# Kernel tuning notes

Hardware: AMD Instinct MI355X
Metric: run time of the kernel (lower is better)

The kernel has to match this reference:

```python
import jax, jax.numpy as jnp
import numpy as np

DEPTH = 4
EPS = 1e-5


def _bn(x, g, b):
    # training-mode BatchNorm over (B,H,W) per channel
    m = x.mean(axis=(0, 2, 3), keepdims=True)
    v = x.var(axis=(0, 2, 3), keepdims=True)
    return (x - m) * jax.lax.rsqrt(v + EPS) * g[None, :, None, None] + b[None, :, None, None]


def _conv_bn(x, w, g, b):
    # 1x1 conv (no bias) + BatchNorm
    y = jnp.einsum('bchw,oc->bohw', x, w)
    return _bn(y, g, b)


def _block_max_broadcast(x, gsz):
    # max over each (H/gsz, W/gsz) block of a gsz x gsz grid, broadcast back
    B, C, H, W = x.shape
    xr = x.reshape(B, C, gsz, H // gsz, gsz, W // gsz)
    m = xr.max(axis=(3, 5), keepdims=True)
    return jnp.broadcast_to(m, xr.shape).reshape(B, C, H, W)


def setup_inputs() -> dict:
    key = jax.random.key(0)
    ks = jax.random.split(key, 3)
    B, C, H, W = 4, 128, 256, 256
    x = jax.random.normal(ks[0], (B, C, H, W), dtype=jnp.float32)
    conv_w = jax.random.normal(ks[1], (DEPTH, C, C), dtype=jnp.float32) * 0.05
    conv_g = jnp.ones((DEPTH, C), dtype=jnp.float32)
    conv_b = jnp.zeros((DEPTH, C), dtype=jnp.float32)
    final_w = jax.random.normal(ks[2], (C, (DEPTH + 1) * C), dtype=jnp.float32) * 0.05
    final_g = jnp.ones((C,), dtype=jnp.float32)
    final_b = jnp.zeros((C,), dtype=jnp.float32)
    return {"x": x, "conv_w": conv_w, "conv_g": conv_g, "conv_b": conv_b,
            "final_w": final_w, "final_g": final_g, "final_b": final_b}


def reference(x, conv_w, conv_g, conv_b, final_w, final_g, final_b):
    # p[0]: identity; p[1+d]: block-max over 2^d x 2^d grid broadcast back, then 1x1 conv+BN
    p = [x]
    for d in range(DEPTH):
        pooled = _block_max_broadcast(x, 2 ** d)  # d=0 -> global max broadcast
        p.append(_conv_bn(pooled, conv_w[d], conv_g[d], conv_b[d]))
    out = jnp.concatenate(p, axis=1)  # [B, 5C, H, W]
    return _conv_bn(out, final_w, final_g, final_b)
```

## Files before the change

kernel.cpp:

```cpp
#include <hip/hip_runtime.h>
#include <hip/hip_bf16.h>
#include <math.h>
#include <float.h>

#define B_ 4
#define C_ 128
#define P_ 65536

#define M3_OFF      0
#define M2_OFF      32768
#define M1_OFF      40960
#define M0_OFF      43008
#define YBASE_      43520
#define SCALED_OFF  87040
#define SHIFTD_OFF  87552
#define CONTRIB_OFF 88064
#define S3_OFF      120832
#define SX_OFF      153600
#define G_OFF       154112
#define SCALEF_OFF  219648
#define SHIFTF_OFF  219776
#define MAXP_OFF    219904
#define SUMP_OFF    744192

using short8 = __attribute__((ext_vector_type(8))) short;
using f32x4 = __attribute__((ext_vector_type(4))) float;
using f32x16 = __attribute__((ext_vector_type(16))) float;

__device__ __forceinline__ int level_rel(int d) {
    return YBASE_ - 512 * (((1 << (2 * (d + 1))) - 1) / 3);
}

__device__ __forceinline__ unsigned int bfpair(float a, float b) {
    union { __hip_bfloat162 h2; unsigned int u; } cv;
    cv.h2 = __float22bfloat162_rn(make_float2(a, b));
    return cv.u;
}

#define GLDS16(src, dst)                                                    \
    __builtin_amdgcn_global_load_lds(                                       \
        (const __attribute__((address_space(1))) unsigned int*)(src),       \
        (__attribute__((address_space(3))) unsigned int*)(dst), 16, 0, 0)

__global__ __launch_bounds__(512, 4) void k_gram_pool(const float* __restrict__ x,
                                                      float* __restrict__ ws,
                                                      float* __restrict__ gpart) {
    __shared__ float buf[4][4096];
    int wg = blockIdx.x;
    int b = wg >> 7, rc = wg & 127;
    const float* xb = x + (size_t)b * C_ * P_ + (size_t)rc * 512;
    int t_ = threadIdx.x, l = t_ & 63, wv = t_ >> 6;
    int qi = wv & 3;
    int qjb = (wv >> 2) * 2;
    bool doacc = (wv < 4);
    int lrow = l >> 3, lch = l & 7;

    f32x16 acc[2];
#pragma unroll
    for (int j = 0; j < 2; ++j)
#pragma unroll
        for (int r = 0; r < 16; ++r) acc[j][r] = 0.f;
    float mxA[8], smA[8];
#pragma unroll
    for (int j = 0; j < 8; ++j) { mxA[j] = -FLT_MAX; smA[j] = 0.f; }

#define ISSUE(tt)                                                            \
    do {                                                                     \
        _Pragma("unroll") for (int i_ = 0; i_ < 2; ++i_) {                   \
            int row_ = wv * 16 + i_ * 8 + lrow;                              \
            int ch_ = lch ^ (row_ & 7);                                      \
            GLDS16(xb + (size_t)row_ * P_ + (tt) * 32 + ch_ * 4,             \
                   &buf[(tt) & 3][(wv * 16 + i_ * 8) * 32]);                 \
        }                                                                    \
    } while (0)

    ISSUE(0);
    ISSUE(1);
    ISSUE(2);

#pragma unroll
    for (int t = 0; t < 16; ++t) {
        if (t <= 13)
            asm volatile("s_waitcnt vmcnt(4)" ::: "memory");
        else if (t == 14)
            asm volatile("s_waitcnt vmcnt(2)" ::: "memory");
        else
            asm volatile("s_waitcnt vmcnt(0)" ::: "memory");
        __builtin_amdgcn_sched_barrier(0);
        __builtin_amdgcn_s_barrier();
        asm volatile("" ::: "memory");
        __builtin_amdgcn_sched_barrier(0);
        if (t + 3 < 16) ISSUE(t + 3);

        const float* tl = &buf[t & 3][0];
        int jc = t & 7;
#pragma unroll
        for (int ks = 0; ks < 2; ++ks) {
            int ch = ks * 4 + ((l >> 5) << 1);
            short8 fa;
            {
                int row = qi * 32 + (l & 31);
                int sw = row & 7;
                float4 v0 = *(const float4*)(tl + row * 32 + ((ch ^ sw) << 2));
                float4 v1 = *(const float4*)(tl + row * 32 + (((ch + 1) ^ sw) << 2));
                if (doacc) {
                    mxA[jc] = fmaxf(mxA[jc],
                        fmaxf(fmaxf(fmaxf(v0.x, v0.y), fmaxf(v0.z, v0.w)),
                              fmaxf(fmaxf(v1.x, v1.y), fmaxf(v1.z, v1.w))));
                    smA[jc] += ((v0.x + v0.y) + (v0.z + v0.w)) +
                               ((v1.x + v1.y) + (v1.z + v1.w));
                }
                union { uint4 u; short8 s8; } cu;
                cu.u = make_uint4(bfpair(v0.x, v0.y), bfpair(v0.z, v0.w),
                                  bfpair(v1.x, v1.y), bfpair(v1.z, v1.w));
                fa = cu.s8;
            }
#pragma unroll
            for (int j = 0; j < 2; ++j) {
                int row = (qjb + j) * 32 + (l & 31);
                int sw = row & 7;
                float4 v0 = *(const float4*)(tl + row * 32 + ((ch ^ sw) << 2));
                float4 v1 = *(const float4*)(tl + row * 32 + (((ch + 1) ^ sw) << 2));
                union { uint4 u; short8 s8; } cu;
                cu.u = make_uint4(bfpair(v0.x, v0.y), bfpair(v0.z, v0.w),
                                  bfpair(v1.x, v1.y), bfpair(v1.z, v1.w));
                acc[j] = __builtin_amdgcn_mfma_f32_32x32x16_bf16(fa, cu.s8, acc[j], 0, 0, 0);
            }
        }
    }
#undef ISSUE

    size_t gb = (size_t)wg * 16384;
#pragma unroll
    for (int j = 0; j < 2; ++j)
#pragma unroll
        for (int r = 0; r < 16; ++r) {
            int row = qi * 32 + (r & 3) + 8 * (r >> 2) + 4 * (l >> 5);
            int col = (qjb + j) * 32 + (l & 31);
            gpart[gb + (size_t)row * 128 + col] = acc[j][r];
        }
    if (doacc) {
        int i3 = rc >> 4, rr = rc & 15;
#pragma unroll
        for (int jc = 0; jc < 8; ++jc) {
            float m = mxA[jc], sv = smA[jc];
            m = fmaxf(m, __shfl_xor(m, 32));
            sv += __shfl_xor(sv, 32);
            if (l < 32) {
                int c = qi * 32 + l;
                size_t idx = ((size_t)(b * 128 + c) * 64 + i3 * 8 + jc) * 16 + rr;
                ws[MAXP_OFF + idx] = m;
                ws[SUMP_OFF + idx] = sv;
            }
        }
    }
}

__global__ __launch_bounds__(256) void k_reduceG(const float* __restrict__ gpart,
                                                 float* __restrict__ ws) {
    int tid = blockIdx.x * 256 + threadIdx.x;
    int b = tid >> 14, inner = tid & 16383;
    const float* p = gpart + (size_t)b * 128 * 16384 + inner;
    float s = 0.f;
    for (int r = 0; r < 128; ++r) s += p[(size_t)r * 16384];
    ws[G_OFF + tid] = s;
}

__global__ __launch_bounds__(256) void k_reduceMS(float* __restrict__ ws) {
    int bc = blockIdx.x;
    int t = threadIdx.x;
    int blk = t >> 2, q = t & 3;
    __shared__ float bm[64], bs[64];
    __shared__ float lv[24];
    __shared__ float sxr[8];
    {
        size_t base = (size_t)bc * 1024 + blk * 16 + q * 4;
        float4 mv = *(const float4*)(ws + MAXP_OFF + base);
        float4 sv = *(const float4*)(ws + SUMP_OFF + base);
        float m = fmaxf(fmaxf(mv.x, mv.y), fmaxf(mv.z, mv.w));
        float s = (sv.x + sv.y) + (sv.z + sv.w);
        m = fmaxf(m, __shfl_xor(m, 1)); s += __shfl_xor(s, 1);
        m = fmaxf(m, __shfl_xor(m, 2)); s += __shfl_xor(s, 2);
        if (q == 0) {
            bm[blk] = m;
            bs[blk] = s;
            ws[M3_OFF + (size_t)bc * 64 + blk] = m;
            ws[S3_OFF + (size_t)bc * 64 + blk] = s;
        }
    }
    __syncthreads();
    if (t < 8) {
        float sx = 0.f;
        for (int r = 0; r < 8; ++r) sx += bs[t * 8 + r];
        sxr[t] = sx;
    }
    if (t < 16) {
        int i2 = t >> 2, j2 = t & 3;
        float m = -FLT_MAX;
        for (int a = 0; a < 2; ++a)
            for (int b2 = 0; b2 < 2; ++b2)
                m = fmaxf(m, bm[(2 * i2 + a) * 8 + 2 * j2 + b2]);
        lv[t] = m;
        ws[M2_OFF + (size_t)bc * 16 + t] = m;
    }
    __syncthreads();
    if (t == 0) {
        float sx = 0.f;
        for (int r = 0; r < 8; ++r) sx += sxr[r];
        ws[SX_OFF + bc] = sx;
    }
    if (t < 4) {
        int i1 = t >> 1, j1 = t & 1;
        float m = -FLT_MAX;
        for (int a = 0; a < 2; ++a)
            for (int b2 = 0; b2 < 2; ++b2)
                m = fmaxf(m, lv[(2 * i1 + a) * 4 + 2 * j1 + b2]);
        lv[16 + t] = m;
        ws[M1_OFF + (size_t)bc * 4 + t] = m;
    }
    __syncthreads();
    if (t == 0)
        ws[M0_OFF + bc] = fmaxf(fmaxf(lv[16], lv[17]), fmaxf(lv[18], lv[19]));
}

__global__ __launch_bounds__(256) void k_conv_pool(const float* __restrict__ conv_w,
                                                   float* __restrict__ ws) {
    int bid = blockIdx.x;
    int d = bid >> 4, b = (bid >> 2) & 3, cchunk = bid & 3;
    int NB = 1 << (2 * d);
    int rel = level_rel(d);
    const float* Mb = ws + rel + (size_t)b * 128 * NB;
    float* Yb = ws + YBASE_ + rel + (size_t)b * 128 * NB;
    __shared__ float mlds[8192];
    int t = threadIdx.x;
    int tot = 128 * NB;
    for (int i = t; i < tot; i += 256) mlds[i] = Mb[i];
    __syncthreads();
    if (NB >= 4) {
        int nbq = NB >> 2;
        int nq = 32 * nbq;
        for (int qi = t; qi < nq; qi += 256) {
            int co = cchunk * 32 + (qi >> (2 * d - 2));
            int bq = qi & (nbq - 1);
            const float* wrow = conv_w + ((size_t)d * 128 + co) * 128;
            float a0 = 0.f, a1 = 0.f, a2 = 0.f, a3 = 0.f;
            for (int ci = 0; ci < 128; ++ci) {
                float4 mv = *(const float4*)(&mlds[ci * NB + bq * 4]);
                float wvv = wrow[ci];
                a0 = fmaf(wvv, mv.x, a0);
                a1 = fmaf(wvv, mv.y, a1);
                a2 = fmaf(wvv, mv.z, a2);
                a3 = fmaf(wvv, mv.w, a3);
            }
            float4 r;
            r.x = a0; r.y = a1; r.z = a2; r.w = a3;
            *(float4*)(&Yb[co * NB + bq * 4]) = r;
        }
    } else {
        for (int oi = t; oi < 32; oi += 256) {
            int co = cchunk * 32 + oi;
            const float* wrow = conv_w + (size_t)co * 128;
            float acc = 0.f;
            for (int ci = 0; ci < 128; ++ci) acc = fmaf(mlds[ci], wrow[ci], acc);
            Yb[co] = acc;
        }
    }
}

__global__ __launch_bounds__(256) void k_bnstats_d(const float* __restrict__ conv_g,
                                                   const float* __restrict__ conv_b,
                                                   float* __restrict__ ws) {
    int tid = blockIdx.x * 256 + threadIdx.x;
    if (tid >= 512) return;
    int d = tid >> 7, c = tid & 127;
    int NB = 1 << (2 * d);
    const float* Y = ws + YBASE_ + level_rel(d);
    int n = 4 * NB;
    float s = 0.f;
    for (int b = 0; b < 4; ++b)
        for (int k = 0; k < NB; ++k) s += Y[((size_t)b * 128 + c) * NB + k];
    float mean = s / (float)n;
    float v = 0.f;
    for (int b = 0; b < 4; ++b)
        for (int k = 0; k < NB; ++k) {
            float dd = Y[((size_t)b * 128 + c) * NB + k] - mean;
            v = fmaf(dd, dd, v);
        }
    float var = v / (float)n;
    float sc = conv_g[d * 128 + c] * rsqrtf(var + 1e-5f);
    ws[SCALED_OFF + tid] = sc;
    ws[SHIFTD_OFF + tid] = conv_b[d * 128 + c] - mean * sc;
}

__global__ __launch_bounds__(128) void k_contrib(const float* __restrict__ final_w,
                                                 float* __restrict__ ws) {
    int b = blockIdx.x >> 6, blk3 = blockIdx.x & 63;
    int i3 = blk3 >> 3, j3 = blk3 & 7;
    __shared__ float pn[512];
    int t = threadIdx.x;
    for (int k = t; k < 512; k += 128) {
        int d = k >> 7, c = k & 127;
        int sh = 3 - d;
        int blkd = (i3 >> sh) * (1 << d) + (j3 >> sh);
        int NB = 1 << (2 * d);
        float yv = ws[YBASE_ + level_rel(d) + ((size_t)b * 128 + c) * NB + blkd];
        pn[k] = yv * ws[SCALED_OFF + k] + ws[SHIFTD_OFF + k];
    }
    __syncthreads();
    const float* fw = final_w + (size_t)t * 640 + 128;
    float acc = 0.f;
#pragma unroll 8
    for (int k = 0; k < 512; k += 4) {
        float4 f = *(const float4*)(fw + k);
        acc = fmaf(pn[k], f.x, acc);
        acc = fmaf(pn[k + 1], f.y, acc);
        acc = fmaf(pn[k + 2], f.z, acc);
        acc = fmaf(pn[k + 3], f.w, acc);
    }
    ws[CONTRIB_OFF + ((size_t)b * 128 + t) * 64 + blk3] = acc;
}

__global__ __launch_bounds__(128) void k_stats(const float* __restrict__ final_w,
                                               const float* __restrict__ final_g,
                                               const float* __restrict__ final_b,
                                               float* __restrict__ ws) {
    int o = blockIdx.x, t = threadIdx.x;
    __shared__ __align__(16) float wlds[128];
    __shared__ __align__(16) float cvl[64];
    __shared__ float rbuf[4];
    wlds[t] = final_w[(size_t)o * 640 + t];
    __syncthreads();
    float SSQ = 0.f, SUM = 0.f;
    for (int b = 0; b < 4; ++b) {
        if (t < 64) cvl[t] = ws[CONTRIB_OFF + (size_t)(b * 128 + o) * 64 + t];
        __syncthreads();
        const float* Gb = ws + G_OFF + (size_t)b * 16384 + (size_t)t * 128;
        float a1 = 0.f;
#pragma unroll 8
        for (int k = 0; k < 128; k += 4) {
            float4 g = *(const float4*)(Gb + k);
            float4 w = *(const float4*)(&wlds[k]);
            a1 = fmaf(g.x, w.x, fmaf(g.y, w.y, fmaf(g.z, w.z, fmaf(g.w, w.w, a1))));
        }
        const float* S3p = ws + S3_OFF + (size_t)(b * 128 + t) * 64;
        float a2 = 0.f;
#pragma unroll 8
        for (int k = 0; k < 64; k += 4) {
            float4 sv = *(const float4*)(S3p + k);
            float4 cv = *(const float4*)(&cvl[k]);
            a2 = fmaf(sv.x, cv.x, fmaf(sv.y, cv.y, fmaf(sv.z, cv.z, fmaf(sv.w, cv.w, a2))));
        }
        float r1 = (a1 + 2.f * a2) * wlds[t];
        float r2 = wlds[t] * ws[SX_OFF + b * 128 + t];
        if (t < 64) {
            r1 += 1024.f * cvl[t] * cvl[t];
            r2 += 1024.f * cvl[t];
        }
#pragma unroll
        for (int k = 1; k < 64; k <<= 1) {
            r1 += __shfl_xor(r1, k);
            r2 += __shfl_xor(r2, k);
        }
        if ((t & 63) == 0) {
            rbuf[(t >> 6) * 2] = r1;
            rbuf[(t >> 6) * 2 + 1] = r2;
        }
        __syncthreads();
        SSQ += rbuf[0] + rbuf[2];
        SUM += rbuf[1] + rbuf[3];
        __syncthreads();
    }
    if (t == 0) {
        float mean = SUM / 262144.f;
        float var = SSQ / 262144.f - mean * mean;
        float sc = final_g[o] * rsqrtf(var + 1e-5f);
        ws[SCALEF_OFF + o] = sc;
        ws[SHIFTF_OFF + o] = final_b[o] - mean * sc;
    }
}

__global__ __launch_bounds__(256) void k_out(const float* __restrict__ x,
                                             const float* __restrict__ final_w,
                                             const float* __restrict__ ws,
                                             float* __restrict__ out) {
    __shared__ uint4 wtileq[2048];
    __shared__ float scl[128], shf[128], cvs[512];
    unsigned char* wtile = (unsigned char*)wtileq;
    int wgid = blockIdx.x;
    int b = wgid >> 9, pt = wgid & 511;
    int p0 = pt * 128;
    int t = threadIdx.x, l = t & 63, wv = t >> 6;
#pragma unroll
    for (int it = 0; it < 32; ++it) {
        int pid = it * 256 + t;
        int o = pid >> 6, cp = (pid & 63) * 2;
        float2 f = *(const float2*)(final_w + (size_t)o * 640 + cp);
        unsigned int u = bfpair(f.x, f.y);
        int wa = (o * 256 + cp * 2) ^ ((o & 7) << 4);
        *(unsigned int*)(wtile + wa) = u;
    }
    if (t < 128) {
        scl[t] = ws[SCALEF_OFF + t];
        shf[t] = ws[SHIFTF_OFF + t];
    }
    int i3 = pt >> 6, jb = (pt & 1) * 4;
    for (int q = t; q < 512; q += 256) {
        int o = q >> 2, jj = q & 3;
        cvs[q] = ws[CONTRIB_OFF + (size_t)(b * 128 + o) * 64 + i3 * 8 + jb + jj];
    }
    __syncthreads();

    const float* xb = x + (size_t)b * C_ * P_;
    int pw = p0 + wv * 32;
    f32x4 acc[8][2];
#pragma unroll
    for (int i = 0; i < 8; ++i) {
        acc[i][0] = (f32x4){0.f, 0.f, 0.f, 0.f};
        acc[i][1] = (f32x4){0.f, 0.f, 0.f, 0.f};
    }
#pragma unroll
    for (int ks = 0; ks < 4; ++ks) {
        short8 bf[2];
#pragma unroll
        for (int nt = 0; nt < 2; ++nt) {
            const float* xp = xb + (size_t)(ks * 32 + (l >> 4) * 8) * P_ + (pw + nt * 16 + (l & 15));
            float f0 = xp[0 * P_], f1 = xp[1 * P_], f2 = xp[2 * P_], f3 = xp[3 * P_];
            float f4 = xp[4 * P_], f5 = xp[5 * P_], f6 = xp[6 * P_], f7 = xp[7 * P_];
            union { uint4 u; short8 s; } cvtu;
            cvtu.u = make_uint4(bfpair(f0, f1), bfpair(f2, f3), bfpair(f4, f5), bfpair(f6, f7));
            bf[nt] = cvtu.s;
        }
#pragma unroll
        for (int mt = 0; mt < 8; ++mt) {
            int ra = ((mt * 16 + (l & 15)) * 256 + ks * 64 + (l >> 4) * 16) ^ ((l & 7) << 4);
            short8 af = *(const short8*)(wtile + ra);
            acc[mt][0] = __builtin_amdgcn_mfma_f32_16x16x32_bf16(af, bf[0], acc[mt][0], 0, 0, 0);
            acc[mt][1] = __builtin_amdgcn_mfma_f32_16x16x32_bf16(af, bf[1], acc[mt][1], 0, 0, 0);
        }
    }
#pragma unroll
    for (int mt = 0; mt < 8; ++mt)
#pragma unroll
        for (int nt = 0; nt < 2; ++nt) {
            int p = pw + nt * 16 + (l & 15);
            int jj = ((p & 255) >> 5) & 3;
#pragma unroll
            for (int r = 0; r < 4; ++r) {
                int o = mt * 16 + (l >> 4) * 4 + r;
                float z = acc[mt][nt][r] + cvs[o * 4 + jj];
                out[(size_t)(b * 128 + o) * P_ + p] = fmaf(z, scl[o], shf[o]);
            }
        }
}

extern "C" void kernel_launch(void* const* d_in, const int* in_sizes, int n_in,
                              void* d_out, int out_size, void* d_ws, size_t ws_size,
                              hipStream_t stream) {
    const float* x = (const float*)d_in[0];
    const float* conv_w = (const float*)d_in[1];
    const float* conv_g = (const float*)d_in[2];
    const float* conv_b = (const float*)d_in[3];
    const float* final_w = (const float*)d_in[4];
    const float* final_g = (const float*)d_in[5];
    const float* final_b = (const float*)d_in[6];
    float* out = (float*)d_out;
    float* ws = (float*)d_ws;

    k_gram_pool<<<512, 512, 0, stream>>>(x, ws, out);
    k_reduceG<<<256, 256, 0, stream>>>(out, ws);
    k_reduceMS<<<512, 256, 0, stream>>>(ws);
    k_conv_pool<<<64, 256, 0, stream>>>(conv_w, ws);
    k_bnstats_d<<<2, 256, 0, stream>>>(conv_g, conv_b, ws);
    k_contrib<<<B_ * 64, 128, 0, stream>>>(final_w, ws);
    k_stats<<<128, 128, 0, stream>>>(final_w, final_g, final_b, ws);
    k_out<<<2048, 256, 0, stream>>>(x, final_w, ws, out);
}
```

Baseline: 194.0 us.

## Convert tiles to bf16 once in registers before LDS staging in gram kernel

Replaces the async global-to-LDS fp32 pipeline with register loads that compute max/sum and convert to bf16 once, then store swizzled bf16 tiles into a double-buffered LDS. MFMA operands are read straight from LDS as short8, removing the repeated fp32 reads and bf16 conversions that every wave performed for its A and B fragments. The tile per phase grows to 128 columns (4 phases instead of 16), using register prefetch for overlap, which raises register pressure and drops the deeper async prefetch.

```diff
diff --git a/kernel.cpp b/kernel.cpp
--- a/kernel.cpp
+++ b/kernel.cpp
@@ -37,98 +37,78 @@
     return cv.u;
 }
 
-#define GLDS16(src, dst)                                                    \
-    __builtin_amdgcn_global_load_lds(                                       \
-        (const __attribute__((address_space(1))) unsigned int*)(src),       \
-        (__attribute__((address_space(3))) unsigned int*)(dst), 16, 0, 0)
-
 __global__ __launch_bounds__(512, 4) void k_gram_pool(const float* __restrict__ x,
                                                       float* __restrict__ ws,
                                                       float* __restrict__ gpart) {
-    __shared__ float buf[4][4096];
+    __shared__ __align__(16) unsigned short buf[2][16384];
     int wg = blockIdx.x;
     int b = wg >> 7, rc = wg & 127;
     const float* xb = x + (size_t)b * C_ * P_ + (size_t)rc * 512;
     int t_ = threadIdx.x, l = t_ & 63, wv = t_ >> 6;
     int qi = wv & 3;
     int qjb = (wv >> 2) * 2;
-    bool doacc = (wv < 4);
-    int lrow = l >> 3, lch = l & 7;
+    int srow = wv * 16 + (l >> 2);
+    int sq = l & 3;
+    const float* sp = xb + (size_t)srow * P_ + sq * 32;
 
     f32x16 acc[2];
 #pragma unroll
     for (int j = 0; j < 2; ++j)
 #pragma unroll
         for (int r = 0; r < 16; ++r) acc[j][r] = 0.f;
-    float mxA[8], smA[8];
-#pragma unroll
-    for (int j = 0; j < 8; ++j) { mxA[j] = -FLT_MAX; smA[j] = 0.f; }
-
-#define ISSUE(tt)                                                            \
+    float mxcb[2] = {-FLT_MAX, -FLT_MAX};
+    float smcb[2] = {0.f, 0.f};
+    float4 ld[8];
+
+#define SLOAD(ph)                                                            \
     do {                                                                     \
-        _Pragma("unroll") for (int i_ = 0; i_ < 2; ++i_) {                   \
-            int row_ = wv * 16 + i_ * 8 + lrow;                              \
-            int ch_ = lch ^ (row_ & 7);                                      \
-            GLDS16(xb + (size_t)row_ * P_ + (tt) * 32 + ch_ * 4,             \
-                   &buf[(tt) & 3][(wv * 16 + i_ * 8) * 32]);                 \
+        _Pragma("unroll") for (int k_ = 0; k_ < 8; ++k_)                     \
+            ld[k_] = *(const float4*)(sp + (ph) * 128 + k_ * 4);             \
+    } while (0)
+#define SSTORE(ph)                                                           \
+    do {                                                                     \
+        _Pragma("unroll") for (int k_ = 0; k_ < 8; ++k_) {                   \
+            float4 v_ = ld[k_];                                              \
+            mxcb[(ph) & 1] = fmaxf(mxcb[(ph) & 1],                           \
+                fmaxf(fmaxf(v_.x, v_.y), fmaxf(v_.z, v_.w)));                \
+            smcb[(ph) & 1] += (v_.x + v_.y) + (v_.z + v_.w);                 \
+        }                                                                    \
+        _Pragma("unroll") for (int k_ = 0; k_ < 4; ++k_) {                   \
+            uint4 u_ = make_uint4(                                           \
+                bfpair(ld[2 * k_].x, ld[2 * k_].y),                          \
+                bfpair(ld[2 * k_].z, ld[2 * k_].w),                          \
+                bfpair(ld[2 * k_ + 1].x, ld[2 * k_ + 1].y),                  \
+                bfpair(ld[2 * k_ + 1].z, ld[2 * k_ + 1].w));                 \
+            int ch_ = (sq * 4 + k_) ^ (srow & 7);                            \
+            *(uint4*)(&buf[(ph) & 1][srow * 128 + ch_ * 8]) = u_;            \
         }                                                                    \
     } while (0)
 
-    ISSUE(0);
-    ISSUE(1);
-    ISSUE(2);
-
-#pragma unroll
-    for (int t = 0; t < 16; ++t) {
-        if (t <= 13)
-            asm volatile("s_waitcnt vmcnt(4)" ::: "memory");
-        else if (t == 14)
-            asm volatile("s_waitcnt vmcnt(2)" ::: "memory");
-        else
-            asm volatile("s_waitcnt vmcnt(0)" ::: "memory");
-        __builtin_amdgcn_sched_barrier(0);
-        __builtin_amdgcn_s_barrier();
-        asm volatile("" ::: "memory");
-        __builtin_amdgcn_sched_barrier(0);
-        if (t + 3 < 16) ISSUE(t + 3);
-
-        const float* tl = &buf[t & 3][0];
-        int jc = t & 7;
-#pragma unroll
-        for (int ks = 0; ks < 2; ++ks) {
-            int ch = ks * 4 + ((l >> 5) << 1);
-            short8 fa;
-            {
-                int row = qi * 32 + (l & 31);
-                int sw = row & 7;
-                float4 v0 = *(const float4*)(tl + row * 32 + ((ch ^ sw) << 2));
-                float4 v1 = *(const float4*)(tl + row * 32 + (((ch + 1) ^ sw) << 2));
-                if (doacc) {
-                    mxA[jc] = fmaxf(mxA[jc],
-                        fmaxf(fmaxf(fmaxf(v0.x, v0.y), fmaxf(v0.z, v0.w)),
-                              fmaxf(fmaxf(v1.x, v1.y), fmaxf(v1.z, v1.w))));
-                    smA[jc] += ((v0.x + v0.y) + (v0.z + v0.w)) +
-                               ((v1.x + v1.y) + (v1.z + v1.w));
-                }
-                union { uint4 u; short8 s8; } cu;
-                cu.u = make_uint4(bfpair(v0.x, v0.y), bfpair(v0.z, v0.w),
-                                  bfpair(v1.x, v1.y), bfpair(v1.z, v1.w));
-                fa = cu.s8;
+    SLOAD(0);
+    SSTORE(0);
+    __syncthreads();
+
+#pragma unroll
+    for (int ph = 0; ph < 4; ++ph) {
+        if (ph < 3) SLOAD(ph + 1);
+        const unsigned short* tl = buf[ph & 1];
+#pragma unroll
+        for (int ks = 0; ks < 8; ++ks) {
+            int ch = ks * 2 + (l >> 5);
+            int rowa = qi * 32 + (l & 31);
+            short8 fa = *(const short8*)(tl + rowa * 128 + ((ch ^ (rowa & 7)) * 8));
+#pragma unroll
+            for (int j = 0; j < 2; ++j) {
+                int rowb = (qjb + j) * 32 + (l & 31);
+                short8 fb = *(const short8*)(tl + rowb * 128 + ((ch ^ (rowb & 7)) * 8));
+                acc[j] = __builtin_amdgcn_mfma_f32_32x32x16_bf16(fa, fb, acc[j], 0, 0, 0);
             }
-#pragma unroll
-            for (int j = 0; j < 2; ++j) {
-                int row = (qjb + j) * 32 + (l & 31);
-                int sw = row & 7;
-                float4 v0 = *(const float4*)(tl + row * 32 + ((ch ^ sw) << 2));
-                float4 v1 = *(const float4*)(tl + row * 32 + (((ch + 1) ^ sw) << 2));
-                union { uint4 u; short8 s8; } cu;
-                cu.u = make_uint4(bfpair(v0.x, v0.y), bfpair(v0.z, v0.w),
-                                  bfpair(v1.x, v1.y), bfpair(v1.z, v1.w));
-                acc[j] = __builtin_amdgcn_mfma_f32_32x32x16_bf16(fa, cu.s8, acc[j], 0, 0, 0);
-            }
-        }
-    }
-#undef ISSUE
+        }
+        if (ph < 3) SSTORE(ph + 1);
+        __syncthreads();
+    }
+#undef SLOAD
+#undef SSTORE
 
     size_t gb = (size_t)wg * 16384;
 #pragma unroll
@@ -139,19 +119,14 @@
             int col = (qjb + j) * 32 + (l & 31);
             gpart[gb + (size_t)row * 128 + col] = acc[j][r];
         }
-    if (doacc) {
+    {
         int i3 = rc >> 4, rr = rc & 15;
 #pragma unroll
-        for (int jc = 0; jc < 8; ++jc) {
-            float m = mxA[jc], sv = smA[jc];
-            m = fmaxf(m, __shfl_xor(m, 32));
-            sv += __shfl_xor(sv, 32);
-            if (l < 32) {
-                int c = qi * 32 + l;
-                size_t idx = ((size_t)(b * 128 + c) * 64 + i3 * 8 + jc) * 16 + rr;
-                ws[MAXP_OFF + idx] = m;
-                ws[SUMP_OFF + idx] = sv;
-            }
+        for (int h = 0; h < 2; ++h) {
+            int cb = h * 4 + sq;
+            size_t idx = ((size_t)(b * 128 + srow) * 64 + i3 * 8 + cb) * 16 + rr;
+            ws[MAXP_OFF + idx] = mxcb[h];
+            ws[SUMP_OFF + idx] = smcb[h];
         }
     }
 }
```

After: 260.3 us. 1.34x slower.

## Split gram-pool work into twice as many workgroups with double buffering

Applied to the files above, without the earlier changes.

Halves the pixel span each k_gram_pool workgroup handles, doubling the grid to 1024 workgroups and raising the occupancy hint to 8. The 4-stage LDS ring with hand-tuned vmcnt waits is replaced by a 2-buffer scheme synchronised with __syncthreads. The aim is more parallelism and latency hiding through occupancy rather than deep per-block prefetch. In exchange the per-block partial Gram matrices double in number, which adds global write traffic and doubles the reduction work in k_reduceG. The pooling partial layout and k_reduceMS are updated to the new span.

```diff
diff --git a/kernel.cpp b/kernel.cpp
--- a/kernel.cpp
+++ b/kernel.cpp
@@ -21,7 +21,7 @@
 #define SCALEF_OFF  219648
 #define SHIFTF_OFF  219776
 #define MAXP_OFF    219904
-#define SUMP_OFF    744192
+#define SUMP_OFF    1268480
 
 using short8 = __attribute__((ext_vector_type(8))) short;
 using f32x4 = __attribute__((ext_vector_type(4))) float;
@@ -42,13 +42,13 @@
         (const __attribute__((address_space(1))) unsigned int*)(src),       \
         (__attribute__((address_space(3))) unsigned int*)(dst), 16, 0, 0)
 
-__global__ __launch_bounds__(512, 4) void k_gram_pool(const float* __restrict__ x,
+__global__ __launch_bounds__(512, 8) void k_gram_pool(const float* __restrict__ x,
                                                       float* __restrict__ ws,
                                                       float* __restrict__ gpart) {
-    __shared__ float buf[4][4096];
+    __shared__ float buf[2][4096];
     int wg = blockIdx.x;
-    int b = wg >> 7, rc = wg & 127;
-    const float* xb = x + (size_t)b * C_ * P_ + (size_t)rc * 512;
+    int b = wg >> 8, rw = wg & 255;
+    const float* xb = x + (size_t)b * C_ * P_ + (size_t)rw * 256;
     int t_ = threadIdx.x, l = t_ & 63, wv = t_ >> 6;
     int qi = wv & 3;
     int qjb = (wv >> 2) * 2;
@@ -70,30 +70,18 @@
             int row_ = wv * 16 + i_ * 8 + lrow;                              \
             int ch_ = lch ^ (row_ & 7);                                      \
             GLDS16(xb + (size_t)row_ * P_ + (tt) * 32 + ch_ * 4,             \
-                   &buf[(tt) & 3][(wv * 16 + i_ * 8) * 32]);                 \
+                   &buf[(tt) & 1][(wv * 16 + i_ * 8) * 32]);                 \
         }                                                                    \
     } while (0)
 
     ISSUE(0);
-    ISSUE(1);
-    ISSUE(2);
-
-#pragma unroll
-    for (int t = 0; t < 16; ++t) {
-        if (t <= 13)
-            asm volatile("s_waitcnt vmcnt(4)" ::: "memory");
-        else if (t == 14)
-            asm volatile("s_waitcnt vmcnt(2)" ::: "memory");
-        else
-            asm volatile("s_waitcnt vmcnt(0)" ::: "memory");
-        __builtin_amdgcn_sched_barrier(0);
-        __builtin_amdgcn_s_barrier();
-        asm volatile("" ::: "memory");
-        __builtin_amdgcn_sched_barrier(0);
-        if (t + 3 < 16) ISSUE(t + 3);
-
-        const float* tl = &buf[t & 3][0];
-        int jc = t & 7;
+    __syncthreads();
+
+#pragma unroll
+    for (int t = 0; t < 8; ++t) {
+        if (t < 7) ISSUE(t + 1);
+        const float* tl = &buf[t & 1][0];
+        int jc = t;
 #pragma unroll
         for (int ks = 0; ks < 2; ++ks) {
             int ch = ks * 4 + ((l >> 5) << 1);
@@ -127,6 +115,7 @@
                 acc[j] = __builtin_amdgcn_mfma_f32_32x32x16_bf16(fa, cu.s8, acc[j], 0, 0, 0);
             }
         }
+        __syncthreads();
     }
 #undef ISSUE
 
@@ -140,7 +129,7 @@
             gpart[gb + (size_t)row * 128 + col] = acc[j][r];
         }
     if (doacc) {
-        int i3 = rc >> 4, rr = rc & 15;
+        int i3 = rw >> 5, rr = rw & 31;
 #pragma unroll
         for (int jc = 0; jc < 8; ++jc) {
             float m = mxA[jc], sv = smA[jc];
@@ -148,7 +137,7 @@
             sv += __shfl_xor(sv, 32);
             if (l < 32) {
                 int c = qi * 32 + l;
-                size_t idx = ((size_t)(b * 128 + c) * 64 + i3 * 8 + jc) * 16 + rr;
+                size_t idx = ((size_t)(b * 128 + c) * 64 + i3 * 8 + jc) * 32 + rr;
                 ws[MAXP_OFF + idx] = m;
                 ws[SUMP_OFF + idx] = sv;
             }
@@ -160,9 +149,9 @@
                                                  float* __restrict__ ws) {
     int tid = blockIdx.x * 256 + threadIdx.x;
     int b = tid >> 14, inner = tid & 16383;
-    const float* p = gpart + (size_t)b * 128 * 16384 + inner;
+    const float* p = gpart + (size_t)b * 256 * 16384 + inner;
     float s = 0.f;
-    for (int r = 0; r < 128; ++r) s += p[(size_t)r * 16384];
+    for (int r = 0; r < 256; ++r) s += p[(size_t)r * 16384];
     ws[G_OFF + tid] = s;
 }
 
@@ -174,11 +163,14 @@
     __shared__ float lv[24];
     __shared__ float sxr[8];
     {
-        size_t base = (size_t)bc * 1024 + blk * 16 + q * 4;
-        float4 mv = *(const float4*)(ws + MAXP_OFF + base);
-        float4 sv = *(const float4*)(ws + SUMP_OFF + base);
-        float m = fmaxf(fmaxf(mv.x, mv.y), fmaxf(mv.z, mv.w));
-        float s = (sv.x + sv.y) + (sv.z + sv.w);
+        size_t base = (size_t)bc * 2048 + blk * 32 + q * 8;
+        float4 m0 = *(const float4*)(ws + MAXP_OFF + base);
+        float4 m1 = *(const float4*)(ws + MAXP_OFF + base + 4);
+        float4 s0 = *(const float4*)(ws + SUMP_OFF + base);
+        float4 s1 = *(const float4*)(ws + SUMP_OFF + base + 4);
+        float m = fmaxf(fmaxf(fmaxf(m0.x, m0.y), fmaxf(m0.z, m0.w)),
+                        fmaxf(fmaxf(m1.x, m1.y), fmaxf(m1.z, m1.w)));
+        float s = (((s0.x + s0.y) + (s0.z + s0.w)) + ((s1.x + s1.y) + (s1.z + s1.w)));
         m = fmaxf(m, __shfl_xor(m, 1)); s += __shfl_xor(s, 1);
         m = fmaxf(m, __shfl_xor(m, 2)); s += __shfl_xor(s, 2);
         if (q == 0) {
@@ -466,7 +458,7 @@
     float* out = (float*)d_out;
     float* ws = (float*)d_ws;
 
-    k_gram_pool<<<512, 512, 0, stream>>>(x, ws, out);
+    k_gram_pool<<<1024, 512, 0, stream>>>(x, ws, out);
     k_reduceG<<<256, 256, 0, stream>>>(out, ws);
     k_reduceMS<<<512, 256, 0, stream>>>(ws);
     k_conv_pool<<<64, 256, 0, stream>>>(conv_w, ws);
```

New measurement: 239.6 us. 23.5% more time.
